# Performance work log

Hardware: AMD Instinct MI355X
Metric: run time of the kernel (lower is better)

## Reference

```python
import jax, jax.numpy as jnp
import numpy as np

B, NPG, DEG = 512, 128, 16          # graphs, nodes/graph, out-degree
N = B * NPG                          # 65536 nodes
E = N * DEG                          # 1048576 edges
IN_DIM, HID, HEADS = 11, 32, 4
K1 = int(np.ceil(0.8 * NPG))         # 103 nodes/graph after pool1
K2 = int(np.ceil(0.8 * K1))          # 83 nodes/graph after pool2


def gat_conv(x, src, dst, mask, W, a_s, a_d, b, n_nodes):
    # PyG GATConv (concat=True, add_self_loops=True, eval mode -> no dropout)
    xp = (x @ W).reshape(n_nodes, HEADS, HID)            # [N,H,C]
    as_ = jnp.einsum('nhc,hc->nh', xp, a_s)
    ad_ = jnp.einsum('nhc,hc->nh', xp, a_d)
    loop = jnp.arange(n_nodes)
    s = jnp.concatenate([src, loop])
    d = jnp.concatenate([dst, loop])
    m = jnp.concatenate([mask, jnp.ones(n_nodes, bool)])
    logit = jax.nn.leaky_relu(as_[s] + ad_[d], 0.2)      # [E+N,H]
    logit = jnp.where(m[:, None], logit, -1e9)
    mx = jax.ops.segment_max(logit, d, num_segments=n_nodes)
    ex = jnp.exp(logit - mx[d]) * m[:, None]
    den = jax.ops.segment_sum(ex, d, num_segments=n_nodes)
    alpha = ex / (den[d] + 1e-16)                        # segment softmax over dst
    out = jax.ops.segment_sum(alpha[:, :, None] * xp[s], d, num_segments=n_nodes)
    return out.reshape(n_nodes, HEADS * HID) + b


def topk_pool(x, src, dst, mask, w, npg, k):
    # PyG TopKPooling: score = tanh((x*w).sum(-1)/||w||); keep top ceil(ratio*n) per graph
    nb = x.shape[0] // npg
    score = jnp.tanh((x @ w) / jnp.linalg.norm(w))
    vals, idx = jax.lax.top_k(score.reshape(nb, npg), k)  # [B,k]
    perm = (idx + (jnp.arange(nb) * npg)[:, None]).reshape(-1)
    x_new = x[perm] * vals.reshape(-1, 1)
    remap = jnp.full(nb * npg, -1).at[perm].set(jnp.arange(nb * k))
    ns, nd = remap[src], remap[dst]
    m = mask & (ns >= 0) & (nd >= 0)
    return x_new, jnp.where(m, ns, 0), jnp.where(m, nd, 0), m


def setup_inputs():
    key = jax.random.key(0)
    ks = jax.random.split(key, 24)
    s = 0.05
    x = jax.random.normal(ks[0], (N, IN_DIM), jnp.float32)
    src = jnp.repeat(jnp.arange(N), DEG)
    dst = (src // NPG) * NPG + jax.random.randint(ks[1], (E,), 0, NPG)
    edge_index = jnp.stack([src, dst])
    edge_attr = jax.random.normal(ks[2], (E, 4), jnp.float32)
    batch = jnp.repeat(jnp.arange(B), NPG)
    p = dict(
        W_g1=jax.random.normal(ks[3], (IN_DIM, HEADS * HID), jnp.float32) * s,
        att_src1=jax.random.normal(ks[4], (HEADS, HID), jnp.float32) * s,
        att_dst1=jax.random.normal(ks[5], (HEADS, HID), jnp.float32) * s,
        b_g1=jnp.zeros((HEADS * HID,), jnp.float32),
        W_t1=jax.random.normal(ks[6], (HEADS * HID, HID), jnp.float32) * s,
        b_t1=jnp.zeros((HID,), jnp.float32),
        pool_w1=jax.random.normal(ks[7], (HID,), jnp.float32) * s,
        W_g2=jax.random.normal(ks[8], (HID, HEADS * HID), jnp.float32) * s,
        att_src2=jax.random.normal(ks[9], (HEADS, HID), jnp.float32) * s,
        att_dst2=jax.random.normal(ks[10], (HEADS, HID), jnp.float32) * s,
        b_g2=jnp.zeros((HEADS * HID,), jnp.float32),
        W_t2=jax.random.normal(ks[11], (HEADS * HID, HID), jnp.float32) * s,
        b_t2=jnp.zeros((HID,), jnp.float32),
        pool_w2=jax.random.normal(ks[12], (HID,), jnp.float32) * s,
        W_l1=jax.random.normal(ks[13], (2 * HID, 256), jnp.float32) * s,
        b_l1=jnp.zeros((256,), jnp.float32),
        W_l2=jax.random.normal(ks[14], (256, 1024), jnp.float32) * s,
        b_l2=jnp.zeros((1024,), jnp.float32),
        W_l3=jax.random.normal(ks[15], (1024, 1), jnp.float32) * s,
        b_l3=jnp.zeros((1,), jnp.float32),
    )
    return dict(x=x, edge_index=edge_index, edge_attr=edge_attr, batch=batch, **p)


def reference(x, edge_index, edge_attr, batch,
              W_g1, att_src1, att_dst1, b_g1, W_t1, b_t1, pool_w1,
              W_g2, att_src2, att_dst2, b_g2, W_t2, b_t2, pool_w2,
              W_l1, b_l1, W_l2, b_l2, W_l3, b_l3):
    # edge_attr is ignored (GATConv built without edge_dim); batch is implicit
    # in the fixed equal-size graph layout.  Eval mode -> dropout disabled.
    src, dst = edge_index[0], edge_index[1]
    mask = jnp.ones(E, bool)
    h = jax.nn.relu(gat_conv(x, src, dst, mask, W_g1, att_src1, att_dst1, b_g1, N))
    h = h @ W_t1 + b_t1
    h, src, dst, mask = topk_pool(h, src, dst, mask, pool_w1, NPG, K1)
    h1 = h.reshape(B, K1, HID)
    g1 = jnp.concatenate([h1.max(1), h1.mean(1)], axis=1)   # [B, 2*HID]
    h = jax.nn.relu(gat_conv(h, src, dst, mask, W_g2, att_src2, att_dst2, b_g2, B * K1))
    h = h @ W_t2 + b_t2
    h, src, dst, mask = topk_pool(h, src, dst, mask, pool_w2, K1, K2)
    h2 = h.reshape(B, K2, HID)
    g2 = jnp.concatenate([h2.max(1), h2.mean(1)], axis=1)
    g = g1 + g2
    g = jax.nn.relu(g @ W_l1 + b_l1)
    g = jax.nn.relu(g @ W_l2 + b_l2)
    return g @ W_l3 + b_l3                                   # [B,1]
```

## Files before the change

kernel.cpp:

```cpp
#include <hip/hip_runtime.h>
#include <math.h>

constexpr int NPGc  = 128;
constexpr int NG    = 512;
constexpr int EPGc  = 2048;
constexpr int ETOT  = 1048576;
constexpr int IND   = 11;
constexpr int HIDc  = 32;
constexpr int FD    = 128;
constexpr int K1c   = 103;
constexpr int K2c   = 83;
constexpr int NN    = NG * NPGc;
constexpr int N2c   = NG * K1c;

__device__ __forceinline__ float lrelu(float x){ return fmaxf(x, 0.2f*x); }

template<int KIN>
__device__ void foldDev(const float* __restrict__ Wg, const float* __restrict__ avs,
                        const float* __restrict__ avd, float* __restrict__ S, float* __restrict__ D, int t)
{
    if (t < KIN * 4) {
        int k = t >> 2, h = t & 3;
        float s = 0.f, d = 0.f;
        for (int j = 0; j < HIDc; j++) {
            float w = Wg[k*FD + h*HIDc + j];
            s = fmaf(w, avs[h*HIDc + j], s);
            d = fmaf(w, avd[h*HIDc + j], d);
        }
        S[t] = s; D[t] = d;
    }
}

__global__ __launch_bounds__(256) void k_prep(const int* __restrict__ ei,
    const float* __restrict__ W1g, const float* __restrict__ s1, const float* __restrict__ d1,
    const float* __restrict__ W2g, const float* __restrict__ s2, const float* __restrict__ d2,
    int* __restrict__ csrOff, unsigned char* __restrict__ csrSB,
    float* __restrict__ S1, float* __restrict__ D1, float* __restrict__ S2, float* __restrict__ D2)
{
    int b = blockIdx.x, t = threadIdx.x;
    if (b >= NG) {
        if (b == NG)     foldDev<IND>(W1g, s1, d1, S1, D1, t);
        else             foldDev<HIDc>(W2g, s2, d2, S2, D2, t);
        return;
    }
    int g = b;
    __shared__ int cnt[128], cur[128], offL[129];
    __shared__ unsigned char sbL[EPGc];
    if (t < 128) cnt[t] = 0;
    __syncthreads();
    const int* dstG = ei + ETOT + g * EPGc;
    int dnv[8];
    #pragma unroll
    for (int q = 0; q < 8; q++) {
        int e = t + 256*q;
        dnv[q] = dstG[e] - g * NPGc;
        atomicAdd(&cnt[dnv[q]], 1);
    }
    __syncthreads();
    if (t < 64) {
        int c0 = cnt[2*t], c1 = cnt[2*t + 1], ps = c0 + c1, P = ps;
        #pragma unroll
        for (int dl = 1; dl < 64; dl <<= 1) { int v = __shfl_up(P, dl); if (t >= dl) P += v; }
        int E0 = P - ps;
        offL[2*t] = E0; offL[2*t + 1] = E0 + c0;
        cur[2*t]  = E0; cur[2*t + 1]  = E0 + c0;
        if (t == 63) offL[128] = P;
    }
    __syncthreads();
    #pragma unroll
    for (int q = 0; q < 8; q++) {
        int e = t + 256*q;
        int pos = atomicAdd(&cur[dnv[q]], 1);
        sbL[pos] = (unsigned char)(e >> 4);
    }
    __syncthreads();
    if (t < 128) ((int4*)(csrSB + (size_t)g * EPGc))[t] = ((const int4*)sbL)[t];
    if (t <= NPGc) csrOff[g*132 + t] = offL[t];
}

template<int NNODE, int KIN>
__global__ __launch_bounds__(256) void k_gat(
    const float* __restrict__ xin, const float* __restrict__ Wg,
    const float* __restrict__ WsS, const float* __restrict__ WsD,
    const int* __restrict__ csrOff, const unsigned char* __restrict__ csrSB,
    const float* __restrict__ bias, const float* __restrict__ Wt,
    float* __restrict__ htp)
{
    int g = blockIdx.x, h = blockIdx.y, t = threadIdx.x;
    constexpr int UN = (NNODE*KIN > EPGc ? NNODE*KIN : EPGc);
    __shared__ __align__(16) float xpL[NNODE * 36];
    __shared__ __align__(16) float uni[UN];
    __shared__ __align__(16) unsigned char sbL[EPGc];
    __shared__ float asL[NNODE], adL[NNODE], sfW[NNODE], sDen[NNODE];
    __shared__ int offL[NNODE + 1];
    __shared__ float WL[KIN * 32];
    __shared__ float WsSL[KIN], WsDL[KIN], bL[32];
    __shared__ __align__(16) float WtsL[1024];

    float* xF  = uni;
    float* wEL = uni;

    {
        const float* xg = xin + (size_t)g * NNODE * KIN;
        if constexpr ((KIN & 3) == 0) {
            for (int i = t; i < NNODE * (KIN/4); i += 256)
                ((float4*)xF)[i] = ((const float4*)xg)[i];
        } else {
            for (int i = t; i < NNODE * KIN; i += 256) xF[i] = xg[i];
        }
    }
    for (int i = t; i < KIN * 32; i += 256) { int k = i >> 5, c = i & 31; WL[i] = Wg[k*FD + h*32 + c]; }
    if (t < KIN) { WsSL[t] = WsS[t*4 + h]; WsDL[t] = WsD[t*4 + h]; }
    if (t < 32) bL[t] = bias[h*32 + t];
    if (t <= NNODE) offL[t] = csrOff[g*132 + t];
    if (t < 128) ((int4*)sbL)[t] = ((const int4*)(csrSB + (size_t)g * EPGc))[t];
    ((float4*)WtsL)[t] = ((const float4*)(Wt + h*1024))[t];
    __syncthreads();

    for (int p = t; p < NNODE * 32; p += 256) {
        int n = p >> 5, c = p & 31;
        const float* xr = xF + n * KIN;
        float acc = 0.f;
        #pragma unroll
        for (int k = 0; k < KIN; k++) acc = fmaf(xr[k], WL[k*32 + c], acc);
        xpL[n*36 + c] = acc;
    }
    if (t < NNODE) {
        const float* xr = xF + t * KIN;
        float s = 0.f, d = 0.f;
        #pragma unroll
        for (int k = 0; k < KIN; k++) { float v = xr[k]; s = fmaf(v, WsSL[k], s); d = fmaf(v, WsDL[k], d); }
        asL[t] = s; adL[t] = d;
    }
    __syncthreads();

    if (t < NNODE) {
        float as_n = asL[t], adn = adL[t];
        int lo = offL[t], hi = offL[t + 1];
        float mx = as_n;
        for (int i = lo; i < hi; i++) mx = fmaxf(mx, asL[sbL[i]]);
        float m = lrelu(mx + adn);
        float ws = expf(lrelu(as_n + adn) - m);
        float den = ws;
        for (int i = lo; i < hi; i++) {
            float w = expf(lrelu(asL[sbL[i]] + adn) - m);
            wEL[i] = w; den += w;
        }
        sfW[t] = ws; sDen[t] = den;
    }
    __syncthreads();

    const float4* X4 = (const float4*)xpL;
    float4 rv[4];
    #pragma unroll
    for (int r = 0; r < 4; r++) {
        int p = t + r*256;
        if (p < NNODE * 8) {
            int n = p >> 3, c4 = p & 7;
            float w0 = sfW[n];
            float4 v = X4[n*9 + c4];
            float4 a; a.x = w0*v.x; a.y = w0*v.y; a.z = w0*v.z; a.w = w0*v.w;
            int lo = offL[n], hi = offL[n + 1];
            for (int s = lo; s < hi; s++) {
                int sc = sbL[s]; float w = wEL[s];
                float4 u = X4[sc*9 + c4];
                a.x = fmaf(w, u.x, a.x); a.y = fmaf(w, u.y, a.y);
                a.z = fmaf(w, u.z, a.z); a.w = fmaf(w, u.w, a.w);
            }
            float inv = 1.f / (sDen[n] + 1e-16f);
            rv[r].x = fmaxf(fmaf(a.x, inv, bL[c4*4 + 0]), 0.f);
            rv[r].y = fmaxf(fmaf(a.y, inv, bL[c4*4 + 1]), 0.f);
            rv[r].z = fmaxf(fmaf(a.z, inv, bL[c4*4 + 2]), 0.f);
            rv[r].w = fmaxf(fmaf(a.w, inv, bL[c4*4 + 3]), 0.f);
        }
    }
    __syncthreads();
    {
        float4* X4w = (float4*)xpL;
        #pragma unroll
        for (int r = 0; r < 4; r++) {
            int p = t + r*256;
            if (p < NNODE * 8) X4w[(p>>3)*9 + (p&7)] = rv[r];
        }
    }
    __syncthreads();

    const int n0 = t >> 3, j4 = t & 7;
    float4 a0 = make_float4(0,0,0,0), a1 = a0, a2 = a0, a3 = a0;
    #pragma unroll 8
    for (int c = 0; c < 32; c++) {
        float4 w4 = *(const float4*)&WtsL[c*HIDc + j4*4];
        float r0 = xpL[n0*36 + c];
        a0.x = fmaf(r0, w4.x, a0.x); a0.y = fmaf(r0, w4.y, a0.y);
        a0.z = fmaf(r0, w4.z, a0.z); a0.w = fmaf(r0, w4.w, a0.w);
        if (n0 + 32 < NNODE) {
            float r1 = xpL[(n0+32)*36 + c];
            a1.x = fmaf(r1, w4.x, a1.x); a1.y = fmaf(r1, w4.y, a1.y);
            a1.z = fmaf(r1, w4.z, a1.z); a1.w = fmaf(r1, w4.w, a1.w);
        }
        if (n0 + 64 < NNODE) {
            float r2 = xpL[(n0+64)*36 + c];
            a2.x = fmaf(r2, w4.x, a2.x); a2.y = fmaf(r2, w4.y, a2.y);
            a2.z = fmaf(r2, w4.z, a2.z); a2.w = fmaf(r2, w4.w, a2.w);
        }
        if (n0 + 96 < NNODE) {
            float r3 = xpL[(n0+96)*36 + c];
            a3.x = fmaf(r3, w4.x, a3.x); a3.y = fmaf(r3, w4.y, a3.y);
            a3.z = fmaf(r3, w4.z, a3.z); a3.w = fmaf(r3, w4.w, a3.w);
        }
    }
    {
        size_t base = ((size_t)(g * NNODE + n0) * 4 + h) * 32 + j4 * 4;
        *(float4*)(htp + base) = a0;
        if (n0 + 32 < NNODE) *(float4*)(htp + base + (size_t)32*128) = a1;
        if (n0 + 64 < NNODE) *(float4*)(htp + base + (size_t)64*128) = a2;
        if (n0 + 96 < NNODE) *(float4*)(htp + base + (size_t)96*128) = a3;
    }
}

template<int NIN, int KEEP, bool FIRST>
__global__ __launch_bounds__(256) void k_linpool(
    const float* __restrict__ htp, const float* __restrict__ bt, const float* __restrict__ pw,
    float* __restrict__ xnew, const int* __restrict__ ei,
    int* __restrict__ csrOffW, unsigned char* __restrict__ sbW,
    float* __restrict__ gfeat, const float* __restrict__ gprev,
    const float* __restrict__ W1, const float* __restrict__ b1,
    const float* __restrict__ W2, const float* __restrict__ b2,
    const float* __restrict__ W3, const float* __restrict__ b3,
    float* __restrict__ outp)
{
    int g = blockIdx.x, t = threadIdx.x;
    __shared__ float htL[NIN * 33];
    __shared__ float scoreL[NIN];
    __shared__ int rnkL[NIN];
    __shared__ int cnt[128], cur[128], offL[129];
    __shared__ unsigned char sbL[EPGc];
    __shared__ float gvec[64];
    __shared__ float h1L[256], red[256];

    for (int p = t; p < NIN * 8; p += 256) {
        int n = p >> 3, q = p & 7;
        const float4* row = (const float4*)(htp + (size_t)(g * NIN + n) * 128);
        float4 s = ((const float4*)bt)[q];
        float4 p0 = row[q], p1 = row[8 + q], p2 = row[16 + q], p3 = row[24 + q];
        s.x += p0.x; s.y += p0.y; s.z += p0.z; s.w += p0.w;
        s.x += p1.x; s.y += p1.y; s.z += p1.z; s.w += p1.w;
        s.x += p2.x; s.y += p2.y; s.z += p2.z; s.w += p2.w;
        s.x += p3.x; s.y += p3.y; s.z += p3.z; s.w += p3.w;
        float* d = htL + n*33 + q*4;
        d[0] = s.x; d[1] = s.y; d[2] = s.z; d[3] = s.w;
    }
    __syncthreads();

    float nrm; { float ss = 0.f; for (int k = 0; k < HIDc; k++) { float w = pw[k]; ss = fmaf(w, w, ss); } nrm = sqrtf(ss); }
    if (t < NIN) {
        float dot = 0.f;
        for (int k = 0; k < HIDc; k++) dot = fmaf(htL[t*33 + k], pw[k], dot);
        scoreL[t] = tanhf(dot / nrm);
    }
    __syncthreads();
    if (t < NIN) {
        float si = scoreL[t]; int rank = 0;
        for (int q = 0; q < NIN; q++) {
            float sj = scoreL[q];
            rank += (sj > si || (sj == si && q < t)) ? 1 : 0;
        }
        rnkL[t] = (rank < KEEP) ? rank : -1;
    }
    __syncthreads();
    if constexpr (FIRST) {
        for (int p = t; p < NIN * 32; p += 256) {
            int n = p >> 5, jj = p & 31;
            int rk = rnkL[n];
            if (rk >= 0) xnew[((size_t)g*KEEP + rk)*HIDc + jj] = htL[n*33 + jj] * scoreL[n];
        }
    }
    if (t < HIDc) {
        float mx = -INFINITY, sm = 0.f;
        for (int n = 0; n < NIN; n++) {
            if (rnkL[n] >= 0) { float v = htL[n*33 + t] * scoreL[n]; mx = fmaxf(mx, v); sm += v; }
        }
        float mean = sm / (float)KEEP;
        if constexpr (FIRST) {
            gfeat[(size_t)g*64 + t]      = mx;
            gfeat[(size_t)g*64 + 32 + t] = mean;
        } else {
            gvec[t]      = gprev[(size_t)g*64 + t] + mx;
            gvec[32 + t] = gprev[(size_t)g*64 + 32 + t] + mean;
        }
    }

    if constexpr (FIRST) {
        __syncthreads();
        if (t < 128) cnt[t] = 0;
        __syncthreads();
        const int* dstG = ei + ETOT + g * EPGc;
        int snv[8], dnv[8];
        #pragma unroll
        for (int q = 0; q < 8; q++) {
            int e = t + 256*q;
            int s = rnkL[e >> 4], d = rnkL[dstG[e] - g * NPGc];
            bool ok = (s >= 0 && d >= 0);
            snv[q] = s; dnv[q] = ok ? d : -1;
            if (ok) atomicAdd(&cnt[d], 1);
        }
        __syncthreads();
        if (t < 64) {
            int c0 = cnt[2*t], c1 = cnt[2*t + 1], ps = c0 + c1, P = ps;
            #pragma unroll
            for (int dl = 1; dl < 64; dl <<= 1) { int v = __shfl_up(P, dl); if (t >= dl) P += v; }
            int E0 = P - ps;
            offL[2*t] = E0; offL[2*t + 1] = E0 + c0;
            cur[2*t]  = E0; cur[2*t + 1]  = E0 + c0;
            if (t == 63) offL[128] = P;
        }
        __syncthreads();
        #pragma unroll
        for (int q = 0; q < 8; q++) {
            if (dnv[q] >= 0) {
                int pos = atomicAdd(&cur[dnv[q]], 1);
                sbL[pos] = (unsigned char)snv[q];
            }
        }
        __syncthreads();
        if (t < 128) ((int4*)(sbW + (size_t)g * EPGc))[t] = ((const int4*)sbL)[t];
        if (t <= K1c) csrOffW[g*132 + t] = offL[t];
    } else {
        __syncthreads();
        float a = b1[t];
        #pragma unroll 4
        for (int k = 0; k < 64; k++) a = fmaf(gvec[k], W1[k*256 + t], a);
        h1L[t] = fmaxf(a, 0.f);
        __syncthreads();
        float c0 = b2[t], c1 = b2[t + 256], c2 = b2[t + 512], c3 = b2[t + 768];
        const float* w2c = W2 + t;
        #pragma unroll 4
        for (int i = 0; i < 256; i++) {
            float hv = h1L[i];
            const float* wr = w2c + (size_t)i * 1024;
            c0 = fmaf(hv, wr[0],   c0);
            c1 = fmaf(hv, wr[256], c1);
            c2 = fmaf(hv, wr[512], c2);
            c3 = fmaf(hv, wr[768], c3);
        }
        float p = fmaf(fmaxf(c0, 0.f), W3[t],
                  fmaf(fmaxf(c1, 0.f), W3[t + 256],
                  fmaf(fmaxf(c2, 0.f), W3[t + 512],
                       fmaxf(c3, 0.f) * W3[t + 768])));
        red[t] = p;
        __syncthreads();
        for (int s = 128; s > 0; s >>= 1) { if (t < s) red[t] += red[t + s]; __syncthreads(); }
        if (t == 0) outp[g] = red[0] + b3[0];
    }
}

extern "C" void kernel_launch(void* const* d_in, const int* in_sizes, int n_in,
                              void* d_out, int out_size, void* d_ws, size_t ws_size,
                              hipStream_t stream)
{
    const float* x    = (const float*)d_in[0];
    const int*   ei   = (const int*)  d_in[1];
    const float* W_g1 = (const float*)d_in[4];
    const float* as1w = (const float*)d_in[5];
    const float* ad1w = (const float*)d_in[6];
    const float* b_g1 = (const float*)d_in[7];
    const float* W_t1 = (const float*)d_in[8];
    const float* b_t1 = (const float*)d_in[9];
    const float* pw1  = (const float*)d_in[10];
    const float* W_g2 = (const float*)d_in[11];
    const float* as2w = (const float*)d_in[12];
    const float* ad2w = (const float*)d_in[13];
    const float* b_g2 = (const float*)d_in[14];
    const float* W_t2 = (const float*)d_in[15];
    const float* b_t2 = (const float*)d_in[16];
    const float* pw2  = (const float*)d_in[17];
    const float* W_l1 = (const float*)d_in[18];
    const float* b_l1 = (const float*)d_in[19];
    const float* W_l2 = (const float*)d_in[20];
    const float* b_l2 = (const float*)d_in[21];
    const float* W_l3 = (const float*)d_in[22];
    const float* b_l3 = (const float*)d_in[23];
    float* out = (float*)d_out;

    char* ws = (char*)d_ws;
    size_t off = 0;
    auto alloc = [&](size_t bytes) -> void* {
        void* p = (void*)(ws + off);
        off += ((bytes + 255) / 256) * 256;
        return p;
    };
    float* htp1  = (float*)alloc((size_t)NN * 128 * 4);
    float* htp2  = (float*)alloc((size_t)N2c * 128 * 4);
    float* x2    = (float*)alloc((size_t)N2c * HIDc * 4);
    float* g1    = (float*)alloc((size_t)NG * 64 * 4);
    float* wsS1  = (float*)alloc(64 * 4);
    float* wsD1  = (float*)alloc(64 * 4);
    float* wsS2  = (float*)alloc(128 * 4);
    float* wsD2  = (float*)alloc(128 * 4);
    int*   off1  = (int*)  alloc((size_t)NG * 132 * 4);
    unsigned char* sb1 = (unsigned char*)alloc((size_t)NG * EPGc);
    int*   off2  = (int*)  alloc((size_t)NG * 132 * 4);
    unsigned char* sb2 = (unsigned char*)alloc((size_t)NG * EPGc);

    k_prep<<<NG + 2, 256, 0, stream>>>(ei, W_g1, as1w, ad1w, W_g2, as2w, ad2w,
                                       off1, sb1, wsS1, wsD1, wsS2, wsD2);

    k_gat<NPGc, IND><<<dim3(NG, 4), 256, 0, stream>>>(
        x, W_g1, wsS1, wsD1, off1, sb1, b_g1, W_t1, htp1);

    k_linpool<NPGc, K1c, true><<<NG, 256, 0, stream>>>(
        htp1, b_t1, pw1, x2, ei, off2, sb2, g1, nullptr,
        nullptr, nullptr, nullptr, nullptr, nullptr, nullptr, nullptr);

    k_gat<K1c, HIDc><<<dim3(NG, 4), 256, 0, stream>>>(
        x2, W_g2, wsS2, wsD2, off2, sb2, b_g2, W_t2, htp2);

    k_linpool<K1c, K2c, false><<<NG, 256, 0, stream>>>(
        htp2, b_t2, pw2, nullptr, nullptr, nullptr, nullptr, nullptr, g1,
        W_l1, b_l1, W_l2, b_l2, W_l3, b_l3, out);
}
```

Baseline: 296.1 us.

## Fuse CSR build and attention-weight folding into the GAT kernel

Removes the separate k_prep launch. The first GAT kernel now builds the per-graph destination CSR directly in shared memory, and each GAT block folds the attention vectors into W itself. This drops one kernel launch and the global round trip for the CSR and the folded weights. In exchange, the CSR build runs redundantly in each of the 4 head blocks per graph, and every block recomputes the small fold. It also reuses the sfW and sDen shared buffers as scratch counters.

```diff
diff --git a/kernel.cpp b/kernel.cpp
--- a/kernel.cpp
+++ b/kernel.cpp
@@ -15,73 +15,11 @@
 
 __device__ __forceinline__ float lrelu(float x){ return fmaxf(x, 0.2f*x); }
 
-template<int KIN>
-__device__ void foldDev(const float* __restrict__ Wg, const float* __restrict__ avs,
-                        const float* __restrict__ avd, float* __restrict__ S, float* __restrict__ D, int t)
-{
-    if (t < KIN * 4) {
-        int k = t >> 2, h = t & 3;
-        float s = 0.f, d = 0.f;
-        for (int j = 0; j < HIDc; j++) {
-            float w = Wg[k*FD + h*HIDc + j];
-            s = fmaf(w, avs[h*HIDc + j], s);
-            d = fmaf(w, avd[h*HIDc + j], d);
-        }
-        S[t] = s; D[t] = d;
-    }
-}
-
-__global__ __launch_bounds__(256) void k_prep(const int* __restrict__ ei,
-    const float* __restrict__ W1g, const float* __restrict__ s1, const float* __restrict__ d1,
-    const float* __restrict__ W2g, const float* __restrict__ s2, const float* __restrict__ d2,
-    int* __restrict__ csrOff, unsigned char* __restrict__ csrSB,
-    float* __restrict__ S1, float* __restrict__ D1, float* __restrict__ S2, float* __restrict__ D2)
-{
-    int b = blockIdx.x, t = threadIdx.x;
-    if (b >= NG) {
-        if (b == NG)     foldDev<IND>(W1g, s1, d1, S1, D1, t);
-        else             foldDev<HIDc>(W2g, s2, d2, S2, D2, t);
-        return;
-    }
-    int g = b;
-    __shared__ int cnt[128], cur[128], offL[129];
-    __shared__ unsigned char sbL[EPGc];
-    if (t < 128) cnt[t] = 0;
-    __syncthreads();
-    const int* dstG = ei + ETOT + g * EPGc;
-    int dnv[8];
-    #pragma unroll
-    for (int q = 0; q < 8; q++) {
-        int e = t + 256*q;
-        dnv[q] = dstG[e] - g * NPGc;
-        atomicAdd(&cnt[dnv[q]], 1);
-    }
-    __syncthreads();
-    if (t < 64) {
-        int c0 = cnt[2*t], c1 = cnt[2*t + 1], ps = c0 + c1, P = ps;
-        #pragma unroll
-        for (int dl = 1; dl < 64; dl <<= 1) { int v = __shfl_up(P, dl); if (t >= dl) P += v; }
-        int E0 = P - ps;
-        offL[2*t] = E0; offL[2*t + 1] = E0 + c0;
-        cur[2*t]  = E0; cur[2*t + 1]  = E0 + c0;
-        if (t == 63) offL[128] = P;
-    }
-    __syncthreads();
-    #pragma unroll
-    for (int q = 0; q < 8; q++) {
-        int e = t + 256*q;
-        int pos = atomicAdd(&cur[dnv[q]], 1);
-        sbL[pos] = (unsigned char)(e >> 4);
-    }
-    __syncthreads();
-    if (t < 128) ((int4*)(csrSB + (size_t)g * EPGc))[t] = ((const int4*)sbL)[t];
-    if (t <= NPGc) csrOff[g*132 + t] = offL[t];
-}
-
-template<int NNODE, int KIN>
+template<int NNODE, int KIN, bool BUILD>
 __global__ __launch_bounds__(256) void k_gat(
     const float* __restrict__ xin, const float* __restrict__ Wg,
-    const float* __restrict__ WsS, const float* __restrict__ WsD,
+    const float* __restrict__ avs, const float* __restrict__ avd,
+    const int* __restrict__ ei,
     const int* __restrict__ csrOff, const unsigned char* __restrict__ csrSB,
     const float* __restrict__ bias, const float* __restrict__ Wt,
     float* __restrict__ htp)
@@ -110,11 +48,52 @@
         }
     }
     for (int i = t; i < KIN * 32; i += 256) { int k = i >> 5, c = i & 31; WL[i] = Wg[k*FD + h*32 + c]; }
-    if (t < KIN) { WsSL[t] = WsS[t*4 + h]; WsDL[t] = WsD[t*4 + h]; }
+    if (t < KIN) {
+        float s = 0.f, d = 0.f;
+        for (int j = 0; j < HIDc; j++) {
+            float w = Wg[t*FD + h*HIDc + j];
+            s = fmaf(w, avs[h*HIDc + j], s);
+            d = fmaf(w, avd[h*HIDc + j], d);
+        }
+        WsSL[t] = s; WsDL[t] = d;
+    }
     if (t < 32) bL[t] = bias[h*32 + t];
-    if (t <= NNODE) offL[t] = csrOff[g*132 + t];
-    if (t < 128) ((int4*)sbL)[t] = ((const int4*)(csrSB + (size_t)g * EPGc))[t];
     ((float4*)WtsL)[t] = ((const float4*)(Wt + h*1024))[t];
+
+    if constexpr (BUILD) {
+        int* cnt = (int*)sfW;
+        int* cur = (int*)sDen;
+        if (t < 128) cnt[t] = 0;
+        __syncthreads();
+        const int* dstG = ei + ETOT + g * EPGc;
+        int dnv[8];
+        #pragma unroll
+        for (int q = 0; q < 8; q++) {
+            int e = t + 256*q;
+            dnv[q] = dstG[e] - g * NPGc;
+            atomicAdd(&cnt[dnv[q]], 1);
+        }
+        __syncthreads();
+        if (t < 64) {
+            int c0 = cnt[2*t], c1 = cnt[2*t + 1], ps = c0 + c1, P = ps;
+            #pragma unroll
+            for (int dl = 1; dl < 64; dl <<= 1) { int v = __shfl_up(P, dl); if (t >= dl) P += v; }
+            int E0 = P - ps;
+            offL[2*t] = E0; offL[2*t + 1] = E0 + c0;
+            cur[2*t]  = E0; cur[2*t + 1]  = E0 + c0;
+            if (t == 63) offL[128] = P;
+        }
+        __syncthreads();
+        #pragma unroll
+        for (int q = 0; q < 8; q++) {
+            int e = t + 256*q;
+            int pos = atomicAdd(&cur[dnv[q]], 1);
+            sbL[pos] = (unsigned char)(e >> 4);
+        }
+    } else {
+        if (t <= NNODE) offL[t] = csrOff[g*132 + t];
+        if (t < 128) ((int4*)sbL)[t] = ((const int4*)(csrSB + (size_t)g * EPGc))[t];
+    }
     __syncthreads();
 
     for (int p = t; p < NNODE * 32; p += 256) {
@@ -393,27 +372,18 @@
     float* htp2  = (float*)alloc((size_t)N2c * 128 * 4);
     float* x2    = (float*)alloc((size_t)N2c * HIDc * 4);
     float* g1    = (float*)alloc((size_t)NG * 64 * 4);
-    float* wsS1  = (float*)alloc(64 * 4);
-    float* wsD1  = (float*)alloc(64 * 4);
-    float* wsS2  = (float*)alloc(128 * 4);
-    float* wsD2  = (float*)alloc(128 * 4);
-    int*   off1  = (int*)  alloc((size_t)NG * 132 * 4);
-    unsigned char* sb1 = (unsigned char*)alloc((size_t)NG * EPGc);
     int*   off2  = (int*)  alloc((size_t)NG * 132 * 4);
     unsigned char* sb2 = (unsigned char*)alloc((size_t)NG * EPGc);
 
-    k_prep<<<NG + 2, 256, 0, stream>>>(ei, W_g1, as1w, ad1w, W_g2, as2w, ad2w,
-                                       off1, sb1, wsS1, wsD1, wsS2, wsD2);
-
-    k_gat<NPGc, IND><<<dim3(NG, 4), 256, 0, stream>>>(
-        x, W_g1, wsS1, wsD1, off1, sb1, b_g1, W_t1, htp1);
+    k_gat<NPGc, IND, true><<<dim3(NG, 4), 256, 0, stream>>>(
+        x, W_g1, as1w, ad1w, ei, nullptr, nullptr, b_g1, W_t1, htp1);
 
     k_linpool<NPGc, K1c, true><<<NG, 256, 0, stream>>>(
         htp1, b_t1, pw1, x2, ei, off2, sb2, g1, nullptr,
         nullptr, nullptr, nullptr, nullptr, nullptr, nullptr, nullptr);
 
-    k_gat<K1c, HIDc><<<dim3(NG, 4), 256, 0, stream>>>(
-        x2, W_g2, wsS2, wsD2, off2, sb2, b_g2, W_t2, htp2);
+    k_gat<K1c, HIDc, false><<<dim3(NG, 4), 256, 0, stream>>>(
+        x2, W_g2, as2w, ad2w, nullptr, off2, sb2, b_g2, W_t2, htp2);
 
     k_linpool<K1c, K2c, false><<<NG, 256, 0, stream>>>(
         htp2, b_t2, pw2, nullptr, nullptr, nullptr, nullptr, nullptr, g1,
```

Result: no change. 300.1 us (+1.4%).
